# Kernel tuning notes

Hardware: AMD Instinct MI355X
Metric: run time of the kernel (lower is better)

Reference implementation:

```python
import jax, jax.numpy as jnp
import numpy as np

NUM_STEPS = 10
TEMP = 2.0
EPS = 1e-20
K = 4   # number of codebooks
N = 8   # codes per codebook
E = 16  # code dim


def _grid_flat():
    x = np.linspace(0.0, 1.5, NUM_STEPS)
    g = np.stack(np.meshgrid(x, x, x), axis=-1)  # [10,10,10,3], 'xy' indexing as in torch source
    return jnp.asarray(g.reshape(-1, 3), dtype=jnp.float32)  # [1000, 3]


def _gumbel(key, shape):
    u = jax.random.uniform(key, shape, dtype=jnp.float32)
    return -jnp.log(-jnp.log(u + EPS) + EPS)


def setup_inputs() -> dict:
    key = jax.random.key(0)
    k1, k2, k3, k4, k5 = jax.random.split(key, 5)
    B, S, D = 32, 2048, 64
    inputs = jax.random.normal(k1, (B, S, D), dtype=jnp.float32)
    linear_w = jax.random.normal(k2, (64, 3), dtype=jnp.float32) * 0.5
    linear_b = jax.random.normal(k3, (64,), dtype=jnp.float32) * 0.1
    emb = jax.random.normal(k4, (K * N, E), dtype=jnp.float32)
    emb_spaces = emb / jnp.linalg.norm(emb, axis=-1, keepdims=True)  # F.normalize(p=2, dim=-1)
    lin_ws = jax.random.normal(k5, (K, E, D), dtype=jnp.float32) * (1.0 / np.sqrt(D))
    return {"inputs": inputs, "linear_w": linear_w, "linear_b": linear_b,
            "emb_spaces": emb_spaces, "lin_ws": lin_ws}


def reference(inputs, linear_w, linear_b, emb_spaces, lin_ws):
    B, S, D = inputs.shape
    grid = _grid_flat()                       # [1000, 3]
    vecs = grid @ linear_w.T + linear_b       # [1000, 64]

    kc, kp = jax.random.split(jax.random.key(42))

    # ---- coordinate codebook path ----
    xc = jnp.einsum('bsd,nd->bsn', inputs, vecs)          # [B,S,1000]
    logc = jax.nn.log_softmax(xc, axis=-1)
    log_u_c = jnp.log(jnp.float32(1.0 / NUM_STEPS ** 3))
    # KLDivLoss(log_uniform, logc, log_target=True, batchmean with input.size(0)=1) == full sum
    kl_c = jnp.sum(jnp.exp(logc) * (logc - log_u_c))
    ic = jax.nn.softmax((logc + _gumbel(kc, logc.shape)) / TEMP, axis=-1)
    quantized_coord = jnp.einsum('bsn,nd->bsd', ic, vecs)  # [B,S,64]

    # ---- per-codebook path (all 4 codebooks vectorized; nums are uniform = 8) ----
    h = jnp.einsum('bsd,ked->bske', inputs, lin_ws)        # [B,S,K,E]
    embK = emb_spaces.reshape(K, N, E)                     # contiguous slices of emb_spaces
    xp = jnp.einsum('bske,kne->bskn', h, embK)             # [B,S,K,N]
    logp = jax.nn.log_softmax(xp, axis=-1)
    log_u = jnp.log(jnp.float32(1.0 / N))
    kl_p = jnp.sum(jnp.exp(logp) * (logp - log_u))         # sum over the K per-codebook KLs
    ip = jax.nn.softmax((logp + _gumbel(kp, logp.shape)) / TEMP, axis=-1)
    quantized = jnp.einsum('bskn,kne->bske', ip, embK).reshape(B, S, K * E)  # [B,S,64]

    loss = (kl_c + kl_p) / 5.0
    return (quantized, quantized_coord, loss)
```

## Files before the change

### kernel.cpp

```cpp
#include <hip/hip_runtime.h>
#include <cstdint>

#define NROWS_HALF 32768
#define QC_OFF 4194304
#define LOSS_OFF 8388608

#define U_CH 0
#define U_CL 2048
#define WS_LOSS_BYTE 8192

#define X_STRIDE 68
#define LOG2E 1.4426950408889634f
#define LN2   0.6931471805599453f

typedef short short8 __attribute__((ext_vector_type(8)));
typedef float float4v __attribute__((ext_vector_type(4)));

#define MFMA16(a, b, c) __builtin_amdgcn_mfma_f32_16x16x32_bf16((a), (b), (c), 0, 0, 0)

__device__ uint32_t g_ticket;

__host__ __device__ __forceinline__ void tf2x32(uint32_t k0, uint32_t k1,
                                                uint32_t x0, uint32_t x1,
                                                uint32_t& o0, uint32_t& o1) {
  const uint32_t k2 = k0 ^ k1 ^ 0x1BD11BDAu;
#define TF_R(r) { x0 += x1; x1 = (x1 << (r)) | (x1 >> (32 - (r))); x1 ^= x0; }
  x0 += k0; x1 += k1;
  TF_R(13) TF_R(15) TF_R(26) TF_R(6)
  x0 += k1; x1 += k2 + 1u;
  TF_R(17) TF_R(29) TF_R(16) TF_R(24)
  x0 += k2; x1 += k0 + 2u;
  TF_R(13) TF_R(15) TF_R(26) TF_R(6)
  x0 += k0; x1 += k1 + 3u;
  TF_R(17) TF_R(29) TF_R(16) TF_R(24)
  x0 += k1; x1 += k2 + 4u;
  TF_R(13) TF_R(15) TF_R(26) TF_R(6)
  x0 += k2; x1 += k0 + 5u;
#undef TF_R
  o0 = x0; o1 = x1;
}

__device__ __forceinline__ float neglog_u(uint32_t bits) {
  const uint32_t mant = bits >> 9;
  const float u = __uint_as_float(mant | 0x3f800000u) - 1.0f;
  const float delta = (float)(8388608u - mant) * 1.1920928955078125e-7f;
  float nl;
  if (delta < 0.00390625f) {
    nl = delta + 0.5f * delta * delta + 0.33333333f * delta * delta * delta;
  } else {
    nl = -LN2 * __builtin_amdgcn_logf(u + 1e-20f);
  }
  return nl;
}

__device__ __forceinline__ uint32_t rn16(float f) {
  uint32_t u = __float_as_uint(f);
  return (u + 0x7FFFu + ((u >> 16) & 1u)) >> 16;
}

__device__ __forceinline__ void split2_rn(float f0, float f1, uint32_t& hi, uint32_t& lo) {
  uint32_t h0 = rn16(f0), h1 = rn16(f1);
  hi = h0 | (h1 << 16);
  float l0 = f0 - __uint_as_float(h0 << 16);
  float l1 = f1 - __uint_as_float(h1 << 16);
  lo = rn16(l0) | (rn16(l1) << 16);
}

__device__ __forceinline__ void split8_rn(const float* p, short8& hi, short8& lo) {
  float4 f0 = *(const float4*)p;
  float4 f1 = *(const float4*)(p + 4);
  union { uint32_t u[4]; short8 s; } H, L;
  split2_rn(f0.x, f0.y, H.u[0], L.u[0]);
  split2_rn(f0.z, f0.w, H.u[1], L.u[1]);
  split2_rn(f1.x, f1.y, H.u[2], L.u[2]);
  split2_rn(f1.z, f1.w, H.u[3], L.u[3]);
  hi = H.s; lo = L.s;
}

__device__ __forceinline__ short8 as_s8(uint4 v) {
  union { uint4 u; short8 s; } c; c.u = v; return c.s;
}

__device__ __forceinline__ float4v tile_mfma(const ushort* __restrict__ Vh,
                                             const ushort* __restrict__ Vl,
                                             int nb, const short8* ah, const short8* al) {
  uint4 bh0 = *(const uint4*)(Vh + nb);
  uint4 bl0 = *(const uint4*)(Vl + nb);
  float4v acc = {0.f, 0.f, 0.f, 0.f};
  acc = MFMA16(ah[0], as_s8(bh0), acc);
  acc = MFMA16(ah[0], as_s8(bl0), acc);
  acc = MFMA16(al[0], as_s8(bh0), acc);
  uint4 bh1 = *(const uint4*)(Vh + nb + 32);
  uint4 bl1 = *(const uint4*)(Vl + nb + 32);
  acc = MFMA16(ah[1], as_s8(bh1), acc);
  acc = MFMA16(ah[1], as_s8(bl1), acc);
  acc = MFMA16(al[1], as_s8(bh1), acc);
  return acc;
}

__global__ void setup_kernel(const float* __restrict__ emb, const float* __restrict__ lws,
                             ushort* __restrict__ wsu) {
  int idx = blockIdx.x * 256 + threadIdx.x;
  if (idx < 2048) {
    int m = idx >> 6, c = idx & 63, k = m >> 3;
    float a = 0.f;
    #pragma unroll
    for (int e = 0; e < 16; ++e) a += emb[m * 16 + e] * lws[(k * 16 + e) * 64 + c];
    a *= LOG2E;
    uint32_t h = rn16(a);
    float fl = a - __uint_as_float(h << 16);
    wsu[U_CH + idx] = (ushort)h;
    wsu[U_CL + idx] = (ushort)rn16(fl);
  } else if (idx == 2048) {
    *(float*)((char*)wsu + WS_LOSS_BYTE) = 0.f;
    g_ticket = 0u;
  }
}

__global__ __launch_bounds__(256, 4) void fused_kernel(
    const float* __restrict__ inp, const float* __restrict__ emb,
    const float* __restrict__ lw, const float* __restrict__ lb,
    const ushort* __restrict__ wsu, float* __restrict__ out,
    float* __restrict__ loss_acc,
    uint32_t kc0, uint32_t kc1, uint32_t kp0, uint32_t kp1) {

  __shared__ float x_s[16 * X_STRIDE];
  __shared__ float xp_s[16 * 32];
  __shared__ float sq_s[16 * 32];
  __shared__ float u_s[16 * 3];
  __shared__ float swq_s[96];
  __shared__ float tq_s[16 * 4];
  __shared__ float kl_s;

  const int t = threadIdx.x;
  const int lane = t & 63;
  const int w = t >> 6;
  const int q = lane >> 4;
  const int mn = lane & 15;
  const int g0 = blockIdx.x * 8;

  if (t == 0) kl_s = 0.f;

  const float pw0 = lw[lane * 3 + 0];
  const float pw1 = lw[lane * 3 + 1];
  const float pw2 = lw[lane * 3 + 2];

  #pragma unroll
  for (int it = 0; it < 4; ++it) {
    int rl = it * 4 + w;
    int row = (rl < 8) ? (g0 + rl) : (g0 + rl - 8 + NROWS_HALF);
    float v = inp[row * 64 + lane];
    x_s[rl * X_STRIDE + lane] = v;
    float u0 = v * pw0, u1 = v * pw1, u2 = v * pw2;
    #pragma unroll
    for (int off = 32; off > 0; off >>= 1) {
      u0 += __shfl_xor(u0, off);
      u1 += __shfl_xor(u1, off);
      u2 += __shfl_xor(u2, off);
    }
    if (lane == 0) {
      u_s[rl * 3 + 0] = u0; u_s[rl * 3 + 1] = u1; u_s[rl * 3 + 2] = u2;
    }
  }
  __syncthreads();

  if (t < 48) {
    const int row = t & 15, axis = t >> 4;
    const float ua = u_s[row * 3 + axis];
    const float b = 1.5f * fmaxf(ua, 0.f);
    float S = 0.f, W = 0.f;
    #pragma unroll
    for (int i = 0; i < 10; ++i) {
      float gi = (float)(i * (1.5 / 9.0));
      float lg = (ua * gi - b) * LOG2E;
      float P = __builtin_amdgcn_exp2f(lg);
      S += P; W += lg * P;
      sq_s[row * 32 + axis * 10 + i] = __builtin_amdgcn_sqrtf(P);
    }
    swq_s[axis * 32 + row * 2 + 0] = S;
    swq_s[axis * 32 + row * 2 + 1] = W;
  }

  short8 ah[2], al[2];
  if (w == 0 || w == 3) {
    #pragma unroll
    for (int s = 0; s < 2; ++s)
      split8_rn(&x_s[mn * X_STRIDE + s * 32 + q * 8], ah[s], al[s]);
  }
  __syncthreads();

  if (t < 16) {
    float Sa = swq_s[t * 2], Wa = swq_s[t * 2 + 1];
    float Sb = swq_s[32 + t * 2], Wb = swq_s[32 + t * 2 + 1];
    float Sc = swq_s[64 + t * 2], Wc = swq_s[64 + t * 2 + 1];
    float kl = LN2 * ((Wa * __builtin_amdgcn_rcpf(Sa) +
                       Wb * __builtin_amdgcn_rcpf(Sb) +
                       Wc * __builtin_amdgcn_rcpf(Sc)) -
                      __builtin_amdgcn_logf(Sa * Sb * Sc)) + 6.9077552789821f;
    atomicAdd(&kl_s, kl);
  }

  if (w == 0 || w == 3) {
    const int cti = (w == 0) ? 1 : 0;
    float4v acc = tile_mfma(wsu + U_CH, wsu + U_CL, (cti * 16 + mn) * 64 + q * 8, ah, al);
    #pragma unroll
    for (int r = 0; r < 4; ++r)
      xp_s[(q * 4 + r) * 32 + cti * 16 + mn] = acc[r];
  }

  float T[16];
  #pragma unroll
  for (int z = 0; z < 16; ++z) T[z] = 0.f;

  #pragma unroll
  for (int pp = 0; pp < 2; ++pp) {
    const int p = w + pp * 4;
    const uint32_t jb = (uint32_t)(g0 + p) * 1000u;
    const float* sqL = &sq_s[p * 32];
    const float* sqH = &sq_s[(p + 8) * 32];
    float t0l = 0.f, t1l = 0.f, t2l = 0.f, t3l = 0.f;
    float t0h = 0.f, t1h = 0.f, t2h = 0.f, t3h = 0.f;
    #pragma unroll 2
    for (int it = 0; it < 16; ++it) {
      int c = it * 64 + lane;
      if (c < 1000) {
        uint32_t y0, y1;
        tf2x32(kc0, kc1, jb + (uint32_t)c, jb + (uint32_t)c + 32768000u, y0, y1);
        int d10 = (c * 6554) >> 16;
        int iy  = (c * 656) >> 16;
        int kz  = c - d10 * 10;
        int jx  = d10 - iy * 10;
        float rL = __builtin_amdgcn_rsqf(neglog_u(y0) + 1e-20f);
        float rH = __builtin_amdgcn_rsqf(neglog_u(y1) + 1e-20f);
        float wL = sqL[jx] * sqL[10 + iy] * (sqL[20 + kz] * rL);
        float wH = sqH[jx] * sqH[10 + iy] * (sqH[20 + kz] * rH);
        float fj = (float)jx, fi = (float)iy, fk = (float)kz;
        t0l += wL; t1l += wL * fj; t2l += wL * fi; t3l += wL * fk;
        t0h += wH; t1h += wH * fj; t2h += wH * fi; t3h += wH * fk;
      }
    }
    T[pp * 8 + 0] = t0l; T[pp * 8 + 1] = t1l; T[pp * 8 + 2] = t2l; T[pp * 8 + 3] = t3l;
    T[pp * 8 + 4] = t0h; T[pp * 8 + 5] = t1h; T[pp * 8 + 6] = t2h; T[pp * 8 + 7] = t3h;
  }

  #pragma unroll
  for (int off = 32; off > 0; off >>= 1) {
    #pragma unroll
    for (int z = 0; z < 16; ++z) T[z] += __shfl_xor(T[z], off);
  }
  if (lane == 0) {
    #pragma unroll
    for (int pp = 0; pp < 2; ++pp) {
      int rl = w + pp * 4, rh = rl + 8;
      #pragma unroll
      for (int cmp = 0; cmp < 4; ++cmp) {
        tq_s[rl * 4 + cmp] = T[pp * 8 + cmp];
        tq_s[rh * 4 + cmp] = T[pp * 8 + 4 + cmp];
      }
    }
  }
  __syncthreads();

  {
    const int d = t & 63, rb = t >> 6;
    const float l0 = lw[d * 3 + 0], l1 = lw[d * 3 + 1], l2 = lw[d * 3 + 2];
    const float lbd = lb[d];
    const float stepf = (float)(1.5 / 9.0);
    #pragma unroll
    for (int kk = 0; kk < 4; ++kk) {
      int m = rb + kk * 4;
      float T0v = tq_s[m * 4 + 0], T1v = tq_s[m * 4 + 1];
      float T2v = tq_s[m * 4 + 2], T3v = tq_s[m * 4 + 3];
      float num = (T1v * l0 + T2v * l1 + T3v * l2) * stepf + T0v * lbd;
      int grow = (m < 8) ? (g0 + m) : (g0 + m - 8 + NROWS_HALF);
      out[QC_OFF + grow * 64 + d] = num * __builtin_amdgcn_rcpf(T0v);
    }
  }

  float* q_s = x_s;
  if (lane < 8) {
    const int u_ = w * 8 + lane;
    const int p = u_ >> 2, k = u_ & 3;
    const int rA = p, rB = p + 8;
    float xpA[8], xpB[8];
    #pragma unroll
    for (int n = 0; n < 8; ++n) {
      xpA[n] = xp_s[rA * 32 + k * 8 + n];
      xpB[n] = xp_s[rB * 32 + k * 8 + n];
    }
    float mA = xpA[0], mB = xpB[0];
    #pragma unroll
    for (int n = 1; n < 8; ++n) { mA = fmaxf(mA, xpA[n]); mB = fmaxf(mB, xpB[n]); }
    const uint32_t base = (uint32_t)(g0 + p) * 32u + (uint32_t)k * 8u;
    float s0A = 0.f, s1A = 0.f, s0B = 0.f, s1B = 0.f, swA = 0.f, swB = 0.f;
    float wvA[8], wvB[8];
    #pragma unroll
    for (int n = 0; n < 8; ++n) {
      float eA = __builtin_amdgcn_exp2f(xpA[n] - mA);
      float eB = __builtin_amdgcn_exp2f(xpB[n] - mB);
      s0A += eA; s1A += eA * xpA[n];
      s0B += eB; s1B += eB * xpB[n];
      uint32_t y0, y1;
      tf2x32(kp0, kp1, base + n, base + n + 1048576u, y0, y1);
      wvA[n] = __builtin_amdgcn_exp2f((xpA[n] - mA) * 0.5f) *
               __builtin_amdgcn_rsqf(neglog_u(y0) + 1e-20f);
      wvB[n] = __builtin_amdgcn_exp2f((xpB[n] - mB) * 0.5f) *
               __builtin_amdgcn_rsqf(neglog_u(y1) + 1e-20f);
      swA += wvA[n]; swB += wvB[n];
    }
    atomicAdd(&kl_s,
        LN2 * ((s1A * __builtin_amdgcn_rcpf(s0A) - mA) - __builtin_amdgcn_logf(s0A)) +
        LN2 * ((s1B * __builtin_amdgcn_rcpf(s0B) - mB) - __builtin_amdgcn_logf(s0B)) +
        4.1588830833596715f);
    float invA = __builtin_amdgcn_rcpf(swA), invB = __builtin_amdgcn_rcpf(swB);
    #pragma unroll
    for (int e = 0; e < 16; ++e) {
      float aA = 0.f, aB = 0.f;
      #pragma unroll
      for (int n = 0; n < 8; ++n) {
        float ev = emb[(k * 8 + n) * 16 + e];
        aA += wvA[n] * ev; aB += wvB[n] * ev;
      }
      q_s[rA * X_STRIDE + k * 16 + e] = aA * invA;
      q_s[rB * X_STRIDE + k * 16 + e] = aB * invB;
    }
  }
  __syncthreads();

  #pragma unroll
  for (int it = 0; it < 4; ++it) {
    int idx = it * 256 + t;
    int rl = idx >> 6, c = idx & 63;
    int row = (rl < 8) ? (g0 + rl) : (g0 + rl - 8 + NROWS_HALF);
    out[row * 64 + c] = q_s[rl * X_STRIDE + c];
  }
  if (t == 0) {
    atomicAdd(loss_acc, kl_s);
    __threadfence();
    uint32_t tk = atomicAdd(&g_ticket, 1u);
    if (tk == 4095u) {
      __threadfence();
      out[LOSS_OFF] = atomicAdd(loss_acc, 0.0f) * 0.2f;
    }
  }
}

extern "C" void kernel_launch(void* const* d_in, const int* in_sizes, int n_in,
                              void* d_out, int out_size, void* d_ws, size_t ws_size,
                              hipStream_t stream) {
  const float* inp  = (const float*)d_in[0];
  const float* lw   = (const float*)d_in[1];
  const float* lb   = (const float*)d_in[2];
  const float* emb  = (const float*)d_in[3];
  const float* lws  = (const float*)d_in[4];
  float* out = (float*)d_out;
  ushort* wsu = (ushort*)d_ws;
  float* loss = (float*)((char*)d_ws + WS_LOSS_BYTE);

  uint32_t a0, b0, a1, b1;
  tf2x32(0u, 42u, 0u, 2u, a0, b0);
  tf2x32(0u, 42u, 1u, 3u, a1, b1);
  const uint32_t kc0 = a0, kc1 = a1;
  const uint32_t kp0 = b0, kp1 = b1;

  setup_kernel<<<9, 256, 0, stream>>>(emb, lws, wsu);
  fused_kernel<<<4096, 256, 0, stream>>>(inp, emb, lw, lb, wsu, out, loss,
                                         kc0, kc1, kp0, kp1);
}
```

Baseline: 252.3 us.

## Spread codebook softmax across all threads and pad coordinate grid loop

Rewrites the per-codebook Gumbel-softmax so that all 256 threads each handle one code, using shuffle reductions, instead of only 8 lanes per wave doing 8 codes serially. The embedding table is staged in shared memory so the quantized output projection is split across all threads. The coordinate loop's c<1000 branch is removed by padding the grid factor tables with zero weights and storing index floats as float2. The cost is extra shared memory and an additional barrier, and the padded iterations for c>=1000 now run RNG work whose result is multiplied by zero.

```diff
diff --git a/kernel.cpp b/kernel.cpp
--- a/kernel.cpp
+++ b/kernel.cpp
@@ -126,10 +126,13 @@
 
   __shared__ float x_s[16 * X_STRIDE];
   __shared__ float xp_s[16 * 32];
-  __shared__ float sq_s[16 * 32];
+  __shared__ float2 sq2_s[16 * 36];
   __shared__ float u_s[16 * 3];
   __shared__ float swq_s[96];
   __shared__ float tq_s[16 * 4];
+  __shared__ float emb_s[512];
+  __shared__ float wv_s[512];
+  __shared__ float inv_s[64];
   __shared__ float kl_s;
 
   const int t = threadIdx.x;
@@ -141,6 +144,9 @@
 
   if (t == 0) kl_s = 0.f;
 
+  emb_s[t] = emb[t];
+  emb_s[t + 256] = emb[t + 256];
+
   const float pw0 = lw[lane * 3 + 0];
   const float pw1 = lw[lane * 3 + 1];
   const float pw2 = lw[lane * 3 + 2];
@@ -175,8 +181,10 @@
       float lg = (ua * gi - b) * LOG2E;
       float P = __builtin_amdgcn_exp2f(lg);
       S += P; W += lg * P;
-      sq_s[row * 32 + axis * 10 + i] = __builtin_amdgcn_sqrtf(P);
-    }
+      sq2_s[row * 36 + axis * 12 + i] = make_float2(__builtin_amdgcn_sqrtf(P), (float)i);
+    }
+    sq2_s[row * 36 + axis * 12 + 10] = make_float2(0.f, 10.f);
+    sq2_s[row * 36 + axis * 12 + 11] = make_float2(0.f, 11.f);
     swq_s[axis * 32 + row * 2 + 0] = S;
     swq_s[axis * 32 + row * 2 + 1] = W;
   }
@@ -216,28 +224,27 @@
   for (int pp = 0; pp < 2; ++pp) {
     const int p = w + pp * 4;
     const uint32_t jb = (uint32_t)(g0 + p) * 1000u;
-    const float* sqL = &sq_s[p * 32];
-    const float* sqH = &sq_s[(p + 8) * 32];
+    const float2* sqL = &sq2_s[p * 36];
+    const float2* sqH = &sq2_s[(p + 8) * 36];
     float t0l = 0.f, t1l = 0.f, t2l = 0.f, t3l = 0.f;
     float t0h = 0.f, t1h = 0.f, t2h = 0.f, t3h = 0.f;
     #pragma unroll 2
     for (int it = 0; it < 16; ++it) {
       int c = it * 64 + lane;
-      if (c < 1000) {
-        uint32_t y0, y1;
-        tf2x32(kc0, kc1, jb + (uint32_t)c, jb + (uint32_t)c + 32768000u, y0, y1);
-        int d10 = (c * 6554) >> 16;
-        int iy  = (c * 656) >> 16;
-        int kz  = c - d10 * 10;
-        int jx  = d10 - iy * 10;
-        float rL = __builtin_amdgcn_rsqf(neglog_u(y0) + 1e-20f);
-        float rH = __builtin_amdgcn_rsqf(neglog_u(y1) + 1e-20f);
-        float wL = sqL[jx] * sqL[10 + iy] * (sqL[20 + kz] * rL);
-        float wH = sqH[jx] * sqH[10 + iy] * (sqH[20 + kz] * rH);
-        float fj = (float)jx, fi = (float)iy, fk = (float)kz;
-        t0l += wL; t1l += wL * fj; t2l += wL * fi; t3l += wL * fk;
-        t0h += wH; t1h += wH * fj; t2h += wH * fi; t3h += wH * fk;
-      }
+      uint32_t y0, y1;
+      tf2x32(kc0, kc1, jb + (uint32_t)c, jb + (uint32_t)c + 32768000u, y0, y1);
+      int d10 = (c * 6554) >> 16;
+      int iy  = (c * 656) >> 16;
+      int kz  = c - d10 * 10;
+      int jx  = d10 - iy * 10;
+      float2 a2 = sqL[jx], b2 = sqL[12 + iy], c2 = sqL[24 + kz];
+      float2 aH = sqH[jx], bH = sqH[12 + iy], cH = sqH[24 + kz];
+      float rL = __builtin_amdgcn_rsqf(neglog_u(y0) + 1e-20f);
+      float rH = __builtin_amdgcn_rsqf(neglog_u(y1) + 1e-20f);
+      float wL = a2.x * b2.x * (c2.x * rL);
+      float wH = aH.x * bH.x * (cH.x * rH);
+      t0l += wL; t1l += wL * a2.y; t2l += wL * b2.y; t3l += wL * c2.y;
+      t0h += wH; t1h += wH * a2.y; t2h += wH * b2.y; t3h += wH * c2.y;
     }
     T[pp * 8 + 0] = t0l; T[pp * 8 + 1] = t1l; T[pp * 8 + 2] = t2l; T[pp * 8 + 3] = t3l;
     T[pp * 8 + 4] = t0h; T[pp * 8 + 5] = t1h; T[pp * 8 + 6] = t2h; T[pp * 8 + 7] = t3h;
@@ -277,52 +284,62 @@
     }
   }
 
+  {
+    const int u_ = t >> 3, n = t & 7;
+    const int p = u_ >> 2, k = u_ & 3;
+    const float xpA = xp_s[p * 32 + k * 8 + n];
+    const float xpB = xp_s[(p + 8) * 32 + k * 8 + n];
+    float mA = xpA, mB = xpB;
+    #pragma unroll
+    for (int off = 1; off < 8; off <<= 1) {
+      mA = fmaxf(mA, __shfl_xor(mA, off));
+      mB = fmaxf(mB, __shfl_xor(mB, off));
+    }
+    float eA = __builtin_amdgcn_exp2f(xpA - mA);
+    float eB = __builtin_amdgcn_exp2f(xpB - mB);
+    float s0A = eA, s1A = eA * xpA, s0B = eB, s1B = eB * xpB;
+    const uint32_t base = (uint32_t)(g0 + p) * 32u + (uint32_t)k * 8u;
+    uint32_t y0, y1;
+    tf2x32(kp0, kp1, base + (uint32_t)n, base + (uint32_t)n + 1048576u, y0, y1);
+    float wvA = __builtin_amdgcn_exp2f((xpA - mA) * 0.5f) *
+                __builtin_amdgcn_rsqf(neglog_u(y0) + 1e-20f);
+    float wvB = __builtin_amdgcn_exp2f((xpB - mB) * 0.5f) *
+                __builtin_amdgcn_rsqf(neglog_u(y1) + 1e-20f);
+    float swA = wvA, swB = wvB;
+    #pragma unroll
+    for (int off = 1; off < 8; off <<= 1) {
+      s0A += __shfl_xor(s0A, off);
+      s1A += __shfl_xor(s1A, off);
+      s0B += __shfl_xor(s0B, off);
+      s1B += __shfl_xor(s1B, off);
+      swA += __shfl_xor(swA, off);
+      swB += __shfl_xor(swB, off);
+    }
+    wv_s[u_ * 16 + n] = wvA;
+    wv_s[u_ * 16 + 8 + n] = wvB;
+    if (n == 0) {
+      inv_s[u_ * 2 + 0] = __builtin_amdgcn_rcpf(swA);
+      inv_s[u_ * 2 + 1] = __builtin_amdgcn_rcpf(swB);
+      atomicAdd(&kl_s,
+          LN2 * ((s1A * __builtin_amdgcn_rcpf(s0A) - mA) - __builtin_amdgcn_logf(s0A)) +
+          LN2 * ((s1B * __builtin_amdgcn_rcpf(s0B) - mB) - __builtin_amdgcn_logf(s0B)) +
+          4.1588830833596715f);
+    }
+  }
+  __syncthreads();
+
   float* q_s = x_s;
-  if (lane < 8) {
-    const int u_ = w * 8 + lane;
-    const int p = u_ >> 2, k = u_ & 3;
-    const int rA = p, rB = p + 8;
-    float xpA[8], xpB[8];
-    #pragma unroll
-    for (int n = 0; n < 8; ++n) {
-      xpA[n] = xp_s[rA * 32 + k * 8 + n];
-      xpB[n] = xp_s[rB * 32 + k * 8 + n];
-    }
-    float mA = xpA[0], mB = xpB[0];
-    #pragma unroll
-    for (int n = 1; n < 8; ++n) { mA = fmaxf(mA, xpA[n]); mB = fmaxf(mB, xpB[n]); }
-    const uint32_t base = (uint32_t)(g0 + p) * 32u + (uint32_t)k * 8u;
-    float s0A = 0.f, s1A = 0.f, s0B = 0.f, s1B = 0.f, swA = 0.f, swB = 0.f;
-    float wvA[8], wvB[8];
-    #pragma unroll
-    for (int n = 0; n < 8; ++n) {
-      float eA = __builtin_amdgcn_exp2f(xpA[n] - mA);
-      float eB = __builtin_amdgcn_exp2f(xpB[n] - mB);
-      s0A += eA; s1A += eA * xpA[n];
-      s0B += eB; s1B += eB * xpB[n];
-      uint32_t y0, y1;
-      tf2x32(kp0, kp1, base + n, base + n + 1048576u, y0, y1);
-      wvA[n] = __builtin_amdgcn_exp2f((xpA[n] - mA) * 0.5f) *
-               __builtin_amdgcn_rsqf(neglog_u(y0) + 1e-20f);
-      wvB[n] = __builtin_amdgcn_exp2f((xpB[n] - mB) * 0.5f) *
-               __builtin_amdgcn_rsqf(neglog_u(y1) + 1e-20f);
-      swA += wvA[n]; swB += wvB[n];
-    }
-    atomicAdd(&kl_s,
-        LN2 * ((s1A * __builtin_amdgcn_rcpf(s0A) - mA) - __builtin_amdgcn_logf(s0A)) +
-        LN2 * ((s1B * __builtin_amdgcn_rcpf(s0B) - mB) - __builtin_amdgcn_logf(s0B)) +
-        4.1588830833596715f);
-    float invA = __builtin_amdgcn_rcpf(swA), invB = __builtin_amdgcn_rcpf(swB);
-    #pragma unroll
-    for (int e = 0; e < 16; ++e) {
-      float aA = 0.f, aB = 0.f;
+  {
+    const int r = t >> 4, e = t & 15;
+    const int p = r & 7, h = r >> 3;
+    #pragma unroll
+    for (int k = 0; k < 4; ++k) {
+      const int u_ = p * 4 + k;
+      float aa = 0.f;
       #pragma unroll
-      for (int n = 0; n < 8; ++n) {
-        float ev = emb[(k * 8 + n) * 16 + e];
-        aA += wvA[n] * ev; aB += wvB[n] * ev;
-      }
-      q_s[rA * X_STRIDE + k * 16 + e] = aA * invA;
-      q_s[rB * X_STRIDE + k * 16 + e] = aB * invB;
+      for (int n = 0; n < 8; ++n)
+        aa += wv_s[u_ * 16 + h * 8 + n] * emb_s[(k * 8 + n) * 16 + e];
+      q_s[r * X_STRIDE + k * 16 + e] = aa * inv_s[u_ * 2 + h];
     }
   }
   __syncthreads();
```

New measurement: 231.8 us. -8.1%, faster.
